# Kernel tuning notes

Hardware: AMD Instinct MI355X
Metric: run time of the kernel (lower is better)

## Reference

```python
import jax, jax.numpy as jnp
import numpy as np

N = 30000          # mesh vertices
B = 5 * 16         # p_bins * t_bins geodesic patch bins
NEURONS = [16, 64, 64, 32]


def setup_inputs() -> dict:
    key = jax.random.key(0)
    ks = jax.random.split(key, 7)
    x = jax.random.normal(ks[0], (N, NEURONS[0]), dtype=jnp.float32)
    conn = jax.random.randint(ks[1], (N, B), 0, N)  # per-vertex per-bin source index
    s1 = 1.0 / np.sqrt(NEURONS[0])
    W1 = jax.random.uniform(ks[2], (NEURONS[0], NEURONS[1]), minval=-s1, maxval=s1, dtype=jnp.float32)
    s2 = 1.0 / np.sqrt(B * NEURONS[1])
    Wg1 = jax.random.uniform(ks[3], (B, NEURONS[1], NEURONS[2]), minval=-s2, maxval=s2, dtype=jnp.float32)
    b1 = jax.random.uniform(ks[4], (NEURONS[2],), minval=-s2, maxval=s2, dtype=jnp.float32)
    s3 = 1.0 / np.sqrt(B * NEURONS[2])
    Wg2 = jax.random.uniform(ks[5], (B, NEURONS[2], NEURONS[3]), minval=-s3, maxval=s3, dtype=jnp.float32)
    b2 = jax.random.uniform(ks[6], (NEURONS[3],), minval=-s3, maxval=s3, dtype=jnp.float32)
    return {"x": x, "W1": W1, "Wg1": Wg1, "b1": b1, "Wg2": Wg2, "b2": b2, "conn": conn}


def _geodesic(h, conn, Wg, b):
    # gather geodesic patch: [N, B, C_in], then per-bin contraction
    patches = h[conn]                               # irregular gather
    return jnp.einsum("nbi,bio->no", patches, Wg) + b


def reference(x, W1, Wg1, b1, Wg2, b2, conn):
    h = jax.nn.relu(x @ W1)                         # linear_1 (no bias, l_bias=False)
    h = jax.nn.relu(_geodesic(h, conn, Wg1, b1))    # GC_1 + relu
    res = _geodesic(h, conn, Wg2, b2)               # GC_2
    norm = jnp.linalg.norm(res, axis=-1, keepdims=True)
    return res / norm
```

## Files before the change

### kernel.cpp

```cpp
#include <hip/hip_runtime.h>
#include <stdint.h>
#include <stddef.h>


typedef __attribute__((ext_vector_type(8))) short bf16x8;
typedef __attribute__((ext_vector_type(4))) float f32x4;

#define BINS 80
#define SPLITK 4
#define BPC 20
#define MROWS 128

static __device__ __forceinline__ unsigned short f2bf(float f) {
  union { float f; unsigned int u; } c; c.f = f;
  unsigned int u = c.u;
  return (unsigned short)((u + 0x7FFFu + ((u >> 16) & 1u)) >> 16);
}

template <int N> static __device__ __forceinline__ void wait_vmcnt() {
  if constexpr (N == 12)      asm volatile("s_waitcnt vmcnt(12)" ::: "memory");
  else if constexpr (N == 10) asm volatile("s_waitcnt vmcnt(10)" ::: "memory");
  else if constexpr (N == 6)  asm volatile("s_waitcnt vmcnt(6)" ::: "memory");
  else if constexpr (N == 5)  asm volatile("s_waitcnt vmcnt(5)" ::: "memory");
  else                        asm volatile("s_waitcnt vmcnt(0)" ::: "memory");
}

__global__ __launch_bounds__(256) void k_lin1(const float* __restrict__ x,
                                              const float* __restrict__ W1,
                                              unsigned short* __restrict__ h1b, int n) {
  __shared__ float w1s[16 * 64];
  int tid = threadIdx.x;
  for (int i = tid; i < 16 * 64; i += 256) w1s[i] = W1[i];
  __syncthreads();
  int v = blockIdx.x * 256 + tid;
  if (v >= n) return;
  const float4* xp = (const float4*)(x + (size_t)v * 16);
  float4 x0 = xp[0], x1 = xp[1], x2 = xp[2], x3 = xp[3];
  float xr[16] = {x0.x, x0.y, x0.z, x0.w, x1.x, x1.y, x1.z, x1.w,
                  x2.x, x2.y, x2.z, x2.w, x3.x, x3.y, x3.z, x3.w};
  float acc[64];
#pragma unroll
  for (int o = 0; o < 64; ++o) acc[o] = 0.f;
#pragma unroll
  for (int i = 0; i < 16; ++i) {
    float xi = xr[i];
#pragma unroll
    for (int o = 0; o < 64; ++o) acc[o] = fmaf(xi, w1s[i * 64 + o], acc[o]);
  }
  unsigned short* hr = h1b + (size_t)v * 64;
#pragma unroll
  for (int o8 = 0; o8 < 8; ++o8) {
    bf16x8 pack;
#pragma unroll
    for (int j = 0; j < 8; ++j) pack[j] = (short)f2bf(fmaxf(acc[o8 * 8 + j], 0.f));
    *(bf16x8*)(hr + o8 * 8) = pack;
  }
}

__global__ __launch_bounds__(256) void k_wimg(const float* __restrict__ Wg,
                                              unsigned char* __restrict__ img,
                                              int O, int total) {
  int t = blockIdx.x * 256 + threadIdx.x;
  if (t >= total) return;
  int c = t & 7;
  int o = (t >> 3) % O;
  int b = t / (O * 8);
  int boff = (o * 128 + c * 16) ^ ((o & 7) << 4);
  bf16x8 pack;
#pragma unroll
  for (int j = 0; j < 8; ++j)
    pack[j] = (short)f2bf(Wg[(size_t)(b * 64 + c * 8 + j) * O + o]);
  *(bf16x8*)(img + (size_t)b * (O * 128) + boff) = pack;
}

template <int OT>
__global__ __launch_bounds__(256, 3) void k_geo_sk(const unsigned short* __restrict__ hin,
                                                   const unsigned char* __restrict__ wimg,
                                                   const int* __restrict__ conn,
                                                   float* __restrict__ part, int n) {
  constexpr int TILEB = OT * 16 * 128;
  constexpr int SINSTS = TILEB / 4096;
  constexpr int IPI = 4 + SINSTS;

  __shared__ int conn_s[MROWS * (BPC + 1)];
  __shared__ alignas(16) unsigned char wg_s[4][TILEB];

  const int tid = threadIdx.x;
  const int lane = tid & 63;
  const int wave = tid >> 6;
  const int ln15 = lane & 15;
  const int lq = lane >> 4;
  const int v0 = blockIdx.x * MROWS;
  const int chunk = blockIdx.y;
  const int bin0 = chunk * BPC;

  for (int idx = tid; idx < MROWS * BPC; idx += 256) {
    int v = idx / BPC;
    int c = idx - v * BPC;
    int vv = v0 + v;
    if (vv > n - 1) vv = n - 1;
    conn_s[v * (BPC + 1) + c] = conn[(size_t)vv * BINS + bin0 + c];
  }

  int boffs[OT][2];
#pragma unroll
  for (int ot = 0; ot < OT; ++ot)
#pragma unroll
    for (int s = 0; s < 2; ++s) {
      int o = ot * 16 + ln15;
      boffs[ot][s] = (o * 128 + s * 64 + lq * 16) ^ ((o & 7) << 4);
    }

  const int koff = lq * 8;
  bf16x8 As[3][2][2];
  f32x4 acc[2][OT];
#pragma unroll
  for (int mt = 0; mt < 2; ++mt)
#pragma unroll
    for (int ot = 0; ot < OT; ++ot) acc[mt][ot] = (f32x4){0.f, 0.f, 0.f, 0.f};

  auto issue = [&](int j) {
#pragma unroll
    for (int mt = 0; mt < 2; ++mt) {
      int cidx = conn_s[(wave * 32 + mt * 16 + ln15) * (BPC + 1) + j];
      const unsigned short* arow = hin + (size_t)cidx * 64 + koff;
      As[j % 3][mt][0] = *(const bf16x8*)(arow);
      As[j % 3][mt][1] = *(const bf16x8*)(arow + 32);
    }
    __builtin_amdgcn_sched_barrier(0);
    const unsigned char* src =
        wimg + (size_t)(bin0 + j) * TILEB + wave * (TILEB / 4) + lane * 16;
    unsigned char* dst = &wg_s[j & 3][wave * (TILEB / 4)];
#pragma unroll
    for (int i = 0; i < SINSTS; ++i) {
      __builtin_amdgcn_global_load_lds(
          (const __attribute__((address_space(1))) unsigned int*)(const void*)(src + i * 1024),
          (__attribute__((address_space(3))) unsigned int*)(void*)(dst + i * 1024),
          16, 0, 0);
    }
    __builtin_amdgcn_sched_barrier(0);
  };

  __syncthreads();
  issue(0);
  issue(1);

#pragma unroll
  for (int cb = 0; cb < BPC; ++cb) {
    if (cb + 2 < BPC) issue(cb + 2);
    const int nafter = IPI * ((cb + 1 < BPC ? 1 : 0) + (cb + 2 < BPC ? 1 : 0));
    if (nafter == 2 * IPI)      wait_vmcnt<2 * IPI>();
    else if (nafter == IPI)     wait_vmcnt<IPI>();
    else                        wait_vmcnt<0>();
    __builtin_amdgcn_s_barrier();
    __builtin_amdgcn_sched_barrier(0);

    const unsigned char* wb = wg_s[cb & 3];
#pragma unroll
    for (int ot = 0; ot < OT; ++ot) {
      bf16x8 b0 = *(const bf16x8*)(wb + boffs[ot][0]);
      bf16x8 b1 = *(const bf16x8*)(wb + boffs[ot][1]);
#pragma unroll
      for (int mt = 0; mt < 2; ++mt) {
        acc[mt][ot] = __builtin_amdgcn_mfma_f32_16x16x32_bf16(As[cb % 3][mt][0], b0,
                                                              acc[mt][ot], 0, 0, 0);
        acc[mt][ot] = __builtin_amdgcn_mfma_f32_16x16x32_bf16(As[cb % 3][mt][1], b1,
                                                              acc[mt][ot], 0, 0, 0);
      }
    }
  }

  constexpr int O = OT * 16;
  float* pbase = part + (size_t)chunk * n * O;
#pragma unroll
  for (int mt = 0; mt < 2; ++mt)
#pragma unroll
    for (int ot = 0; ot < OT; ++ot)
#pragma unroll
      for (int r = 0; r < 4; ++r) {
        int v = v0 + wave * 32 + mt * 16 + lq * 4 + r;
        if (v < n) pbase[(size_t)v * O + ot * 16 + ln15] = acc[mt][ot][r];
      }
}

__global__ __launch_bounds__(256) void k_fin1(const float* __restrict__ part,
                                              const float* __restrict__ bias,
                                              unsigned short* __restrict__ out, int n) {
  int t = blockIdx.x * 256 + threadIdx.x;
  int total = n * 16;
  if (t >= total) return;
  int base = t * 4;
  int o = base & 63;
  size_t stride = (size_t)n * 64;
  const float* p = part + base;
  float4 s = *(const float4*)(p);
#pragma unroll
  for (int c = 1; c < SPLITK; ++c) {
    float4 q = *(const float4*)(p + c * stride);
    s.x += q.x; s.y += q.y; s.z += q.z; s.w += q.w;
  }
  float4 b4 = *(const float4*)(bias + o);
  ushort4 pack;
  pack.x = f2bf(fmaxf(s.x + b4.x, 0.f));
  pack.y = f2bf(fmaxf(s.y + b4.y, 0.f));
  pack.z = f2bf(fmaxf(s.z + b4.z, 0.f));
  pack.w = f2bf(fmaxf(s.w + b4.w, 0.f));
  *(ushort4*)(out + base) = pack;
}

__global__ __launch_bounds__(256) void k_fin2(const float* __restrict__ part,
                                              const float* __restrict__ bias,
                                              float* __restrict__ out, int n) {
  int v = blockIdx.x * 16 + (threadIdx.x >> 4);
  int o = threadIdx.x & 15;
  if (v >= n) return;
  size_t stride = (size_t)n * 32;
  const float* p = part + (size_t)v * 32 + o;
  float a = 0.f, b = 0.f;
#pragma unroll
  for (int c = 0; c < SPLITK; ++c) {
    a += p[c * stride];
    b += p[c * stride + 16];
  }
  a += bias[o];
  b += bias[o + 16];
  float ss = a * a + b * b;
  ss += __shfl_xor(ss, 1);
  ss += __shfl_xor(ss, 2);
  ss += __shfl_xor(ss, 4);
  ss += __shfl_xor(ss, 8);
  float inv = 1.0f / sqrtf(ss);
  out[(size_t)v * 32 + o] = a * inv;
  out[(size_t)v * 32 + 16 + o] = b * inv;
}

extern "C" void kernel_launch(void* const* d_in, const int* in_sizes, int n_in,
                              void* d_out, int out_size, void* d_ws, size_t ws_size,
                              hipStream_t stream) {
  const float* x   = (const float*)d_in[0];
  const float* W1  = (const float*)d_in[1];
  const float* Wg1 = (const float*)d_in[2];
  const float* b1  = (const float*)d_in[3];
  const float* Wg2 = (const float*)d_in[4];
  const float* b2  = (const float*)d_in[5];
  const int*  conn = (const int*)d_in[6];
  int n = in_sizes[0] / 16;

  unsigned char* ws = (unsigned char*)d_ws;
  size_t hb = ((size_t)n * 64 * 2 + 255) & ~(size_t)255;
  unsigned short* h1b = (unsigned short*)(ws);
  unsigned short* h2b = (unsigned short*)(ws + hb);
  unsigned char*  w1i = ws + 2 * hb;
  unsigned char*  w2i = ws + 2 * hb + 80 * 8192;
  float* part = (float*)(ws + 2 * hb + 80 * 8192 + 80 * 4096);

  k_wimg<<<(80 * 64 * 8 + 255) / 256, 256, 0, stream>>>(Wg1, w1i, 64, 80 * 64 * 8);
  k_wimg<<<(80 * 32 * 8 + 255) / 256, 256, 0, stream>>>(Wg2, w2i, 32, 80 * 32 * 8);
  k_lin1<<<(n + 255) / 256, 256, 0, stream>>>(x, W1, h1b, n);

  int gb = (n + MROWS - 1) / MROWS;
  k_geo_sk<4><<<dim3(gb, SPLITK), 256, 0, stream>>>(h1b, w1i, conn, part, n);
  k_fin1<<<(n * 16 + 255) / 256, 256, 0, stream>>>(part, b1, h2b, n);
  k_geo_sk<2><<<dim3(gb, SPLITK), 256, 0, stream>>>(h2b, w2i, conn, part, n);
  k_fin2<<<(n + 15) / 16, 256, 0, stream>>>(part, b2, (float*)d_out, n);
}
```

Baseline: 136.7 us.

## Preload all bin weight tiles into LDS and deepen gather prefetch pipeline

Replaces the per-bin weight streaming kernel with one that loads all 20 bins' weight tiles into shared memory once, then runs a barrier-free loop with a 6-deep register prefetch of gathered activation rows. Blocks grow to 512 threads over 256 vertices, and the 64-wide output of layer one is split across a third grid dimension into two 32-column halves. This removes per-iteration barriers and vmcnt waits but uses about 100KB of LDS and more registers, which limits occupancy to one block per CU, and it duplicates the activation gather for the two output halves.

```diff
diff --git a/kernel.cpp b/kernel.cpp
--- a/kernel.cpp
+++ b/kernel.cpp
@@ -9,20 +9,12 @@
 #define BINS 80
 #define SPLITK 4
 #define BPC 20
-#define MROWS 128
+#define PF 6
 
 static __device__ __forceinline__ unsigned short f2bf(float f) {
   union { float f; unsigned int u; } c; c.f = f;
   unsigned int u = c.u;
   return (unsigned short)((u + 0x7FFFu + ((u >> 16) & 1u)) >> 16);
-}
-
-template <int N> static __device__ __forceinline__ void wait_vmcnt() {
-  if constexpr (N == 12)      asm volatile("s_waitcnt vmcnt(12)" ::: "memory");
-  else if constexpr (N == 10) asm volatile("s_waitcnt vmcnt(10)" ::: "memory");
-  else if constexpr (N == 6)  asm volatile("s_waitcnt vmcnt(6)" ::: "memory");
-  else if constexpr (N == 5)  asm volatile("s_waitcnt vmcnt(5)" ::: "memory");
-  else                        asm volatile("s_waitcnt vmcnt(0)" ::: "memory");
 }
 
 __global__ __launch_bounds__(256) void k_lin1(const float* __restrict__ x,
@@ -73,113 +65,110 @@
   *(bf16x8*)(img + (size_t)b * (O * 128) + boff) = pack;
 }
 
-template <int OT>
-__global__ __launch_bounds__(256, 3) void k_geo_sk(const unsigned short* __restrict__ hin,
-                                                   const unsigned char* __restrict__ wimg,
-                                                   const int* __restrict__ conn,
-                                                   float* __restrict__ part, int n) {
-  constexpr int TILEB = OT * 16 * 128;
-  constexpr int SINSTS = TILEB / 4096;
-  constexpr int IPI = 4 + SINSTS;
-
-  __shared__ int conn_s[MROWS * (BPC + 1)];
-  __shared__ alignas(16) unsigned char wg_s[4][TILEB];
+template <int SRCT, int OSTR>
+__global__ __launch_bounds__(512, 1) void k_geo2(const unsigned short* __restrict__ hin,
+                                                 const unsigned char* __restrict__ wimg,
+                                                 const int* __restrict__ conn,
+                                                 float* __restrict__ part, int n) {
+  __shared__ alignas(16) unsigned char wg_s[BPC * 4096];
+  __shared__ int conn_s[256 * BPC];
 
   const int tid = threadIdx.x;
   const int lane = tid & 63;
   const int wave = tid >> 6;
   const int ln15 = lane & 15;
   const int lq = lane >> 4;
-  const int v0 = blockIdx.x * MROWS;
-  const int chunk = blockIdx.y;
-  const int bin0 = chunk * BPC;
-
-  for (int idx = tid; idx < MROWS * BPC; idx += 256) {
-    int v = idx / BPC;
-    int c = idx - v * BPC;
+  const int v0 = blockIdx.x * 256;
+  const int bin0 = blockIdx.y * BPC;
+  const int zh = blockIdx.z;
+
+  for (int t = tid; t < 256 * (BPC / 4); t += 512) {
+    int v = t / (BPC / 4);
+    int c4 = t - v * (BPC / 4);
     int vv = v0 + v;
     if (vv > n - 1) vv = n - 1;
-    conn_s[v * (BPC + 1) + c] = conn[(size_t)vv * BINS + bin0 + c];
-  }
-
-  int boffs[OT][2];
-#pragma unroll
-  for (int ot = 0; ot < OT; ++ot)
+    int4 q = *(const int4*)(conn + (size_t)vv * BINS + bin0 + c4 * 4);
+    *(int4*)(&conn_s[v * BPC + c4 * 4]) = q;
+  }
+
+  {
+    const unsigned char* wsrc = wimg + (size_t)bin0 * SRCT + (size_t)zh * 4096;
+#pragma unroll
+    for (int r = 0; r < 10; ++r) {
+      int off = (r * 512 + tid) * 16;
+      int bin = off >> 12;
+      int within = off & 4095;
+      __builtin_amdgcn_global_load_lds(
+          (const __attribute__((address_space(1))) unsigned int*)(const void*)(wsrc + (size_t)bin * SRCT + within),
+          (__attribute__((address_space(3))) unsigned int*)(void*)(wg_s + off),
+          16, 0, 0);
+    }
+  }
+  __syncthreads();
+
+  int boffs[2][2];
+#pragma unroll
+  for (int ot = 0; ot < 2; ++ot)
 #pragma unroll
     for (int s = 0; s < 2; ++s) {
       int o = ot * 16 + ln15;
       boffs[ot][s] = (o * 128 + s * 64 + lq * 16) ^ ((o & 7) << 4);
     }
 
+  const int crow0 = (wave * 32 + ln15) * BPC;
+  const int crow1 = crow0 + 16 * BPC;
   const int koff = lq * 8;
-  bf16x8 As[3][2][2];
-  f32x4 acc[2][OT];
+
+  bf16x8 As[8][2][2];
+  f32x4 acc[2][2];
 #pragma unroll
   for (int mt = 0; mt < 2; ++mt)
 #pragma unroll
-    for (int ot = 0; ot < OT; ++ot) acc[mt][ot] = (f32x4){0.f, 0.f, 0.f, 0.f};
-
-  auto issue = [&](int j) {
-#pragma unroll
-    for (int mt = 0; mt < 2; ++mt) {
-      int cidx = conn_s[(wave * 32 + mt * 16 + ln15) * (BPC + 1) + j];
-      const unsigned short* arow = hin + (size_t)cidx * 64 + koff;
-      As[j % 3][mt][0] = *(const bf16x8*)(arow);
-      As[j % 3][mt][1] = *(const bf16x8*)(arow + 32);
-    }
-    __builtin_amdgcn_sched_barrier(0);
-    const unsigned char* src =
-        wimg + (size_t)(bin0 + j) * TILEB + wave * (TILEB / 4) + lane * 16;
-    unsigned char* dst = &wg_s[j & 3][wave * (TILEB / 4)];
-#pragma unroll
-    for (int i = 0; i < SINSTS; ++i) {
-      __builtin_amdgcn_global_load_lds(
-          (const __attribute__((address_space(1))) unsigned int*)(const void*)(src + i * 1024),
-          (__attribute__((address_space(3))) unsigned int*)(void*)(dst + i * 1024),
-          16, 0, 0);
-    }
-    __builtin_amdgcn_sched_barrier(0);
-  };
-
-  __syncthreads();
-  issue(0);
-  issue(1);
-
-#pragma unroll
-  for (int cb = 0; cb < BPC; ++cb) {
-    if (cb + 2 < BPC) issue(cb + 2);
-    const int nafter = IPI * ((cb + 1 < BPC ? 1 : 0) + (cb + 2 < BPC ? 1 : 0));
-    if (nafter == 2 * IPI)      wait_vmcnt<2 * IPI>();
-    else if (nafter == IPI)     wait_vmcnt<IPI>();
-    else                        wait_vmcnt<0>();
-    __builtin_amdgcn_s_barrier();
-    __builtin_amdgcn_sched_barrier(0);
-
-    const unsigned char* wb = wg_s[cb & 3];
-#pragma unroll
-    for (int ot = 0; ot < OT; ++ot) {
+    for (int ot = 0; ot < 2; ++ot) acc[mt][ot] = (f32x4){0.f, 0.f, 0.f, 0.f};
+
+#define ISSUE(j)                                                        \
+  {                                                                     \
+    int c0 = conn_s[crow0 + (j)];                                       \
+    int c1 = conn_s[crow1 + (j)];                                       \
+    const unsigned short* r0 = hin + (size_t)c0 * 64 + koff;            \
+    const unsigned short* r1 = hin + (size_t)c1 * 64 + koff;            \
+    As[(j) & 7][0][0] = *(const bf16x8*)(r0);                           \
+    As[(j) & 7][0][1] = *(const bf16x8*)(r0 + 32);                      \
+    As[(j) & 7][1][0] = *(const bf16x8*)(r1);                           \
+    As[(j) & 7][1][1] = *(const bf16x8*)(r1 + 32);                      \
+  }
+
+#pragma unroll
+  for (int j = 0; j < PF; ++j) ISSUE(j);
+
+#pragma unroll
+  for (int b = 0; b < BPC; ++b) {
+    if (b + PF < BPC) ISSUE(b + PF);
+    const unsigned char* wb = wg_s + b * 4096;
+#pragma unroll
+    for (int ot = 0; ot < 2; ++ot) {
       bf16x8 b0 = *(const bf16x8*)(wb + boffs[ot][0]);
       bf16x8 b1 = *(const bf16x8*)(wb + boffs[ot][1]);
 #pragma unroll
       for (int mt = 0; mt < 2; ++mt) {
-        acc[mt][ot] = __builtin_amdgcn_mfma_f32_16x16x32_bf16(As[cb % 3][mt][0], b0,
+        acc[mt][ot] = __builtin_amdgcn_mfma_f32_16x16x32_bf16(As[b & 7][mt][0], b0,
                                                               acc[mt][ot], 0, 0, 0);
-        acc[mt][ot] = __builtin_amdgcn_mfma_f32_16x16x32_bf16(As[cb % 3][mt][1], b1,
+        acc[mt][ot] = __builtin_amdgcn_mfma_f32_16x16x32_bf16(As[b & 7][mt][1], b1,
                                                               acc[mt][ot], 0, 0, 0);
       }
     }
   }
-
-  constexpr int O = OT * 16;
-  float* pbase = part + (size_t)chunk * n * O;
+#undef ISSUE
+
+  float* pbase = part + (size_t)blockIdx.y * n * OSTR + zh * 32;
 #pragma unroll
   for (int mt = 0; mt < 2; ++mt)
 #pragma unroll
-    for (int ot = 0; ot < OT; ++ot)
+    for (int ot = 0; ot < 2; ++ot)
 #pragma unroll
       for (int r = 0; r < 4; ++r) {
         int v = v0 + wave * 32 + mt * 16 + lq * 4 + r;
-        if (v < n) pbase[(size_t)v * O + ot * 16 + ln15] = acc[mt][ot][r];
+        if (v < n) pbase[(size_t)v * OSTR + ot * 16 + ln15] = acc[mt][ot][r];
       }
 }
 
@@ -258,9 +247,9 @@
   k_wimg<<<(80 * 32 * 8 + 255) / 256, 256, 0, stream>>>(Wg2, w2i, 32, 80 * 32 * 8);
   k_lin1<<<(n + 255) / 256, 256, 0, stream>>>(x, W1, h1b, n);
 
-  int gb = (n + MROWS - 1) / MROWS;
-  k_geo_sk<4><<<dim3(gb, SPLITK), 256, 0, stream>>>(h1b, w1i, conn, part, n);
+  int vt = (n + 255) / 256;
+  k_geo2<8192, 64><<<dim3(vt, SPLITK, 2), 512, 0, stream>>>(h1b, w1i, conn, part, n);
   k_fin1<<<(n * 16 + 255) / 256, 256, 0, stream>>>(part, b1, h2b, n);
-  k_geo_sk<2><<<dim3(gb, SPLITK), 256, 0, stream>>>(h2b, w2i, conn, part, n);
+  k_geo2<4096, 32><<<dim3(vt, SPLITK, 1), 512, 0, stream>>>(h2b, w2i, conn, part, n);
   k_fin2<<<(n + 15) / 16, 256, 0, stream>>>(part, b2, (float*)d_out, n);
 }
```

Result: slower. 167.2 us (+22.3%).

## Restructure geodesic kernel into K-half phases with resident weight slabs and deeper gather prefetch

Applied to the files above, without the earlier changes.

The geodesic kernel now uses 512-thread blocks over 256 vertices. It splits the 64-wide input channel dimension into two phases. In each phase all 20 bins' weight half-slabs are staged into LDS once, instead of rotating a 4-deep ring with a barrier every bin. Gathered rows are prefetched 6 bins ahead using inline-asm loads and vmcnt waits. The weight image layout is changed to match, with a rotation swizzle in place of the XOR. This is meant to remove per-bin barriers and hide irregular gather latency. The cost is 1 block per CU, a larger LDS footprint, and two passes over the gathers.

```diff
diff --git a/kernel.cpp b/kernel.cpp
--- a/kernel.cpp
+++ b/kernel.cpp
@@ -9,7 +9,7 @@
 #define BINS 80
 #define SPLITK 4
 #define BPC 20
-#define MROWS 128
+#define PF 6
 
 static __device__ __forceinline__ unsigned short f2bf(float f) {
   union { float f; unsigned int u; } c; c.f = f;
@@ -17,12 +17,14 @@
   return (unsigned short)((u + 0x7FFFu + ((u >> 16) & 1u)) >> 16);
 }
 
-template <int N> static __device__ __forceinline__ void wait_vmcnt() {
-  if constexpr (N == 12)      asm volatile("s_waitcnt vmcnt(12)" ::: "memory");
-  else if constexpr (N == 10) asm volatile("s_waitcnt vmcnt(10)" ::: "memory");
-  else if constexpr (N == 6)  asm volatile("s_waitcnt vmcnt(6)" ::: "memory");
-  else if constexpr (N == 5)  asm volatile("s_waitcnt vmcnt(5)" ::: "memory");
-  else                        asm volatile("s_waitcnt vmcnt(0)" ::: "memory");
+static __device__ __forceinline__ void wait_vm(int m) {
+  if (m >= 12)      asm volatile("s_waitcnt vmcnt(12)");
+  else if (m == 10) asm volatile("s_waitcnt vmcnt(10)");
+  else if (m == 8)  asm volatile("s_waitcnt vmcnt(8)");
+  else if (m == 6)  asm volatile("s_waitcnt vmcnt(6)");
+  else if (m == 4)  asm volatile("s_waitcnt vmcnt(4)");
+  else if (m == 2)  asm volatile("s_waitcnt vmcnt(2)");
+  else              asm volatile("s_waitcnt vmcnt(0)");
 }
 
 __global__ __launch_bounds__(256) void k_lin1(const float* __restrict__ x,
@@ -62,113 +64,121 @@
                                               int O, int total) {
   int t = blockIdx.x * 256 + threadIdx.x;
   if (t >= total) return;
-  int c = t & 7;
-  int o = (t >> 3) % O;
-  int b = t / (O * 8);
-  int boff = (o * 128 + c * 16) ^ ((o & 7) << 4);
+  int j = t & 3;
+  int r = t >> 2;
+  int o = r % O;
+  int r2 = r / O;
+  int z = r2 & 1;
+  int b = r2 >> 1;
   bf16x8 pack;
 #pragma unroll
-  for (int j = 0; j < 8; ++j)
-    pack[j] = (short)f2bf(Wg[(size_t)(b * 64 + c * 8 + j) * O + o]);
-  *(bf16x8*)(img + (size_t)b * (O * 128) + boff) = pack;
+  for (int tt = 0; tt < 8; ++tt)
+    pack[tt] = (short)f2bf(Wg[(size_t)(b * 64 + z * 32 + j * 8 + tt) * O + o]);
+  size_t boff = (size_t)b * (O * 128) + z * (O * 64) + o * 64 + ((j + (o >> 1)) & 3) * 16;
+  *(bf16x8*)(img + boff) = pack;
 }
 
 template <int OT>
-__global__ __launch_bounds__(256, 3) void k_geo_sk(const unsigned short* __restrict__ hin,
-                                                   const unsigned char* __restrict__ wimg,
-                                                   const int* __restrict__ conn,
-                                                   float* __restrict__ part, int n) {
-  constexpr int TILEB = OT * 16 * 128;
-  constexpr int SINSTS = TILEB / 4096;
-  constexpr int IPI = 4 + SINSTS;
-
-  __shared__ int conn_s[MROWS * (BPC + 1)];
-  __shared__ alignas(16) unsigned char wg_s[4][TILEB];
+__global__ __launch_bounds__(512, 1) void k_geo3(const unsigned short* __restrict__ hin,
+                                                 const unsigned char* __restrict__ wimg,
+                                                 const int* __restrict__ conn,
+                                                 float* __restrict__ part, int n) {
+  constexpr int SLAB = OT * 1024;
+  constexpr int R = (BPC * SLAB) / 8192;
+  __shared__ alignas(16) unsigned char wg_s[BPC * SLAB];
+  __shared__ int conn_s[256 * 21];
 
   const int tid = threadIdx.x;
   const int lane = tid & 63;
   const int wave = tid >> 6;
   const int ln15 = lane & 15;
   const int lq = lane >> 4;
-  const int v0 = blockIdx.x * MROWS;
+  const int v0 = blockIdx.x * 256;
   const int chunk = blockIdx.y;
   const int bin0 = chunk * BPC;
 
-  for (int idx = tid; idx < MROWS * BPC; idx += 256) {
-    int v = idx / BPC;
-    int c = idx - v * BPC;
+  for (int t = tid; t < 256 * BPC; t += 512) {
+    int v = t / BPC, c = t - v * BPC;
     int vv = v0 + v;
     if (vv > n - 1) vv = n - 1;
-    conn_s[v * (BPC + 1) + c] = conn[(size_t)vv * BINS + bin0 + c];
-  }
-
-  int boffs[OT][2];
-#pragma unroll
-  for (int ot = 0; ot < OT; ++ot)
-#pragma unroll
-    for (int s = 0; s < 2; ++s) {
-      int o = ot * 16 + ln15;
-      boffs[ot][s] = (o * 128 + s * 64 + lq * 16) ^ ((o & 7) << 4);
-    }
-
-  const int koff = lq * 8;
-  bf16x8 As[3][2][2];
-  f32x4 acc[2][OT];
-#pragma unroll
-  for (int mt = 0; mt < 2; ++mt)
-#pragma unroll
-    for (int ot = 0; ot < OT; ++ot) acc[mt][ot] = (f32x4){0.f, 0.f, 0.f, 0.f};
-
-  auto issue = [&](int j) {
-#pragma unroll
-    for (int mt = 0; mt < 2; ++mt) {
-      int cidx = conn_s[(wave * 32 + mt * 16 + ln15) * (BPC + 1) + j];
-      const unsigned short* arow = hin + (size_t)cidx * 64 + koff;
-      As[j % 3][mt][0] = *(const bf16x8*)(arow);
-      As[j % 3][mt][1] = *(const bf16x8*)(arow + 32);
-    }
-    __builtin_amdgcn_sched_barrier(0);
-    const unsigned char* src =
-        wimg + (size_t)(bin0 + j) * TILEB + wave * (TILEB / 4) + lane * 16;
-    unsigned char* dst = &wg_s[j & 3][wave * (TILEB / 4)];
-#pragma unroll
-    for (int i = 0; i < SINSTS; ++i) {
+    conn_s[v * 21 + c] = conn[(size_t)vv * BINS + bin0 + c];
+  }
+
+  auto stage = [&](int ph) {
+#pragma unroll
+    for (int r = 0; r < R; ++r) {
+      int off = (r * 512 + tid) * 16;
+      int bin = off / SLAB;
+      int within = off & (SLAB - 1);
       __builtin_amdgcn_global_load_lds(
-          (const __attribute__((address_space(1))) unsigned int*)(const void*)(src + i * 1024),
-          (__attribute__((address_space(3))) unsigned int*)(void*)(dst + i * 1024),
+          (const __attribute__((address_space(1))) unsigned int*)(const void*)
+              (wimg + (size_t)(bin0 + bin) * (2 * SLAB) + ph * SLAB + within),
+          (__attribute__((address_space(3))) unsigned int*)(void*)(wg_s + off),
           16, 0, 0);
     }
-    __builtin_amdgcn_sched_barrier(0);
   };
 
-  __syncthreads();
-  issue(0);
-  issue(1);
-
-#pragma unroll
-  for (int cb = 0; cb < BPC; ++cb) {
-    if (cb + 2 < BPC) issue(cb + 2);
-    const int nafter = IPI * ((cb + 1 < BPC ? 1 : 0) + (cb + 2 < BPC ? 1 : 0));
-    if (nafter == 2 * IPI)      wait_vmcnt<2 * IPI>();
-    else if (nafter == IPI)     wait_vmcnt<IPI>();
-    else                        wait_vmcnt<0>();
-    __builtin_amdgcn_s_barrier();
-    __builtin_amdgcn_sched_barrier(0);
-
-    const unsigned char* wb = wg_s[cb & 3];
-#pragma unroll
-    for (int ot = 0; ot < OT; ++ot) {
-      bf16x8 b0 = *(const bf16x8*)(wb + boffs[ot][0]);
-      bf16x8 b1 = *(const bf16x8*)(wb + boffs[ot][1]);
-#pragma unroll
-      for (int mt = 0; mt < 2; ++mt) {
-        acc[mt][ot] = __builtin_amdgcn_mfma_f32_16x16x32_bf16(As[cb % 3][mt][0], b0,
-                                                              acc[mt][ot], 0, 0, 0);
-        acc[mt][ot] = __builtin_amdgcn_mfma_f32_16x16x32_bf16(As[cb % 3][mt][1], b1,
-                                                              acc[mt][ot], 0, 0, 0);
+  int boffs[OT];
+#pragma unroll
+  for (int ot = 0; ot < OT; ++ot) {
+    int o = ot * 16 + ln15;
+    boffs[ot] = o * 64 + ((lq + (o >> 1)) & 3) * 16;
+  }
+
+  const int crow0 = (wave * 32 + ln15) * 21;
+  const int crow1 = crow0 + 16 * 21;
+  const int koff = lq * 8;
+
+  bf16x8 As[8][2];
+  f32x4 acc[2][OT];
+#pragma unroll
+  for (int mt = 0; mt < 2; ++mt)
+#pragma unroll
+    for (int ot = 0; ot < OT; ++ot) acc[mt][ot] = (f32x4){0.f, 0.f, 0.f, 0.f};
+
+#define ISSUE(ph, j) do {                                                        \
+    int c0_ = conn_s[crow0 + (j)];                                               \
+    int c1_ = conn_s[crow1 + (j)];                                               \
+    const void* p0_ = (const void*)(hin + (size_t)c0_ * 64 + (ph) * 32 + koff);  \
+    const void* p1_ = (const void*)(hin + (size_t)c1_ * 64 + (ph) * 32 + koff);  \
+    asm volatile("global_load_dwordx4 %0, %1, off" : "=v"(As[(j) & 7][0]) : "v"(p0_)); \
+    asm volatile("global_load_dwordx4 %0, %1, off" : "=v"(As[(j) & 7][1]) : "v"(p1_)); \
+  } while (0)
+
+  auto run_phase = [&](int ph) {
+#pragma unroll
+    for (int b = 0; b < BPC; ++b) {
+      if (b + PF < BPC) ISSUE(ph, b + PF);
+      int rem = BPC - 1 - b;
+      wait_vm(2 * (rem > PF ? PF : rem));
+      __builtin_amdgcn_sched_barrier(0);
+      const unsigned char* wb = wg_s + b * SLAB;
+#pragma unroll
+      for (int ot = 0; ot < OT; ++ot) {
+        bf16x8 bf = *(const bf16x8*)(wb + boffs[ot]);
+        acc[0][ot] = __builtin_amdgcn_mfma_f32_16x16x32_bf16(As[b & 7][0], bf, acc[0][ot], 0, 0, 0);
+        acc[1][ot] = __builtin_amdgcn_mfma_f32_16x16x32_bf16(As[b & 7][1], bf, acc[1][ot], 0, 0, 0);
       }
     }
-  }
+  };
+
+  stage(0);
+  __syncthreads();
+#pragma unroll
+  for (int j = 0; j < PF; ++j) ISSUE(0, j);
+  run_phase(0);
+
+  asm volatile("s_waitcnt lgkmcnt(0)" ::: "memory");
+  __builtin_amdgcn_s_barrier();
+  __builtin_amdgcn_sched_barrier(0);
+  stage(1);
+#pragma unroll
+  for (int j = 0; j < PF; ++j) ISSUE(1, j);
+  asm volatile("s_waitcnt vmcnt(0)" ::: "memory");
+  __builtin_amdgcn_s_barrier();
+  __builtin_amdgcn_sched_barrier(0);
+  run_phase(1);
+#undef ISSUE
 
   constexpr int O = OT * 16;
   float* pbase = part + (size_t)chunk * n * O;
@@ -254,13 +264,13 @@
   unsigned char*  w2i = ws + 2 * hb + 80 * 8192;
   float* part = (float*)(ws + 2 * hb + 80 * 8192 + 80 * 4096);
 
-  k_wimg<<<(80 * 64 * 8 + 255) / 256, 256, 0, stream>>>(Wg1, w1i, 64, 80 * 64 * 8);
-  k_wimg<<<(80 * 32 * 8 + 255) / 256, 256, 0, stream>>>(Wg2, w2i, 32, 80 * 32 * 8);
+  k_wimg<<<(80 * 2 * 64 * 4 + 255) / 256, 256, 0, stream>>>(Wg1, w1i, 64, 80 * 2 * 64 * 4);
+  k_wimg<<<(80 * 2 * 32 * 4 + 255) / 256, 256, 0, stream>>>(Wg2, w2i, 32, 80 * 2 * 32 * 4);
   k_lin1<<<(n + 255) / 256, 256, 0, stream>>>(x, W1, h1b, n);
 
-  int gb = (n + MROWS - 1) / MROWS;
-  k_geo_sk<4><<<dim3(gb, SPLITK), 256, 0, stream>>>(h1b, w1i, conn, part, n);
+  int vt = (n + 255) / 256;
+  k_geo3<4><<<dim3(vt, SPLITK), 512, 0, stream>>>(h1b, w1i, conn, part, n);
   k_fin1<<<(n * 16 + 255) / 256, 256, 0, stream>>>(part, b1, h2b, n);
-  k_geo_sk<2><<<dim3(gb, SPLITK), 256, 0, stream>>>(h2b, w2i, conn, part, n);
+  k_geo3<2><<<dim3(vt, SPLITK), 512, 0, stream>>>(h2b, w2i, conn, part, n);
   k_fin2<<<(n + 15) / 16, 256, 0, stream>>>(part, b2, (float*)d_out, n);
 }
```

After: 131.7 us. 1.04x faster.
